# Kernel tuning notes

Hardware: AMD Instinct MI355X
Metric: run time of the kernel (lower is better)

## Reference

```python
import jax, jax.numpy as jnp
import numpy as np

RADIUS = 0.2
NSAMPLE = 32


def ball_query(new_xyz, xyz, radius, nsample):
    # new_xyz: (B, M, 3), xyz: (B, N, 3) -> idx: (B, M, nsample) int32
    B, M, _ = new_xyz.shape
    N = xyz.shape[1]
    # pairwise squared distances (B, M, N)
    diff = new_xyz[:, :, None, :] - xyz[:, None, :, :]
    dist2 = jnp.sum(diff * diff, axis=-1)
    mask = dist2 < (radius * radius)
    ar = jnp.arange(N, dtype=jnp.int32)
    masked = jnp.where(mask, ar[None, None, :], jnp.int32(N + 1))  # (B,M,N)
    sorted_idx = jnp.sort(masked, axis=2)[:, :, :nsample]          # (B,M,nsample)
    invalid = sorted_idx >= N
    first = sorted_idx[:, :, 0:1]
    idx = jnp.where(invalid, jnp.broadcast_to(first, sorted_idx.shape), sorted_idx)
    return idx


def group_points(points, idx):
    # points: (B, C, N), idx: (B, M, nsample) -> (B, C, M, nsample)
    B, C, N = points.shape
    M, ns = idx.shape[1], idx.shape[2]
    flat = jnp.broadcast_to(idx.reshape(B, 1, M * ns), (B, C, M * ns))
    return jnp.take_along_axis(points, flat, axis=2).reshape(B, C, M, ns)


def setup_inputs() -> dict:
    key = jax.random.key(0)
    k1, k2, k3 = jax.random.split(key, 3)
    xyz = jax.random.uniform(k1, (8, 16384, 3), dtype=jnp.float32)
    new_xyz = jax.random.uniform(k2, (8, 1024, 3), dtype=jnp.float32)
    features = jax.random.normal(k3, (8, 64, 16384), dtype=jnp.float32)
    return {"xyz": xyz, "new_xyz": new_xyz, "features": features}


def reference(xyz, new_xyz, features):
    idx = ball_query(new_xyz, xyz, RADIUS, NSAMPLE)          # (B,M,ns)
    xyz_t = jnp.transpose(xyz, (0, 2, 1))                    # (B,3,N)
    grouped_xyz = group_points(xyz_t, idx)                   # (B,3,M,ns)
    grouped_xyz = grouped_xyz - jnp.transpose(new_xyz, (0, 2, 1))[:, :, :, None]
    grouped_features = group_points(features, idx)           # (B,C,M,ns)
    new_features = jnp.concatenate([grouped_xyz, grouped_features], axis=1)
    return new_features                                      # (B, 3+C, M, ns)
```

## Files before the change

### kernel.cpp

```cpp
#include <hip/hip_runtime.h>


#define N_PTS   16384
#define M_Q     1024
#define B_SZ    8
#define NSAMP   32
#define NCH     64
#define R2      0.04f
#define OUT_CH  (3 + NCH)

typedef float f4 __attribute__((ext_vector_type(4)));

__global__ __launch_bounds__(256) void transpose_kernel(
    const float* __restrict__ feat, const float* __restrict__ xyz,
    float* __restrict__ ft,
    float* __restrict__ xs, float* __restrict__ ys, float* __restrict__ zs)
{
    __shared__ float tile[64][65];
    const int b   = blockIdx.x & 7;
    const int n0  = (blockIdx.x >> 3) << 6;
    const int tid = threadIdx.x;
    const float* __restrict__ fb = feat + (size_t)b * NCH * N_PTS;
    float* __restrict__ tb       = ft   + ((size_t)b * N_PTS + n0) * NCH;

    if (xs && tid < 64) {
        const int p = n0 + tid;
        const float* src = xyz + ((size_t)b * N_PTS + p) * 3;
        xs[(size_t)b * N_PTS + p] = src[0];
        ys[(size_t)b * N_PTS + p] = src[1];
        zs[(size_t)b * N_PTS + p] = src[2];
    }

#pragma unroll
    for (int j = 0; j < 4; ++j) {
        const int fidx = j * 256 + tid;
        const int c = fidx >> 4;
        const int q = fidx & 15;
        const f4 v = __builtin_nontemporal_load(
            (const f4*)&fb[(size_t)c * N_PTS + n0 + q * 4]);
        tile[c][q * 4 + 0] = v.x;
        tile[c][q * 4 + 1] = v.y;
        tile[c][q * 4 + 2] = v.z;
        tile[c][q * 4 + 3] = v.w;
    }
    __syncthreads();
    const int c4 = tid & 15;
    const int r  = tid >> 4;
#pragma unroll
    for (int j = 0; j < 4; ++j) {
        const int nn = j * 16 + r;
        f4 o;
        o.x = tile[c4 * 4 + 0][nn];
        o.y = tile[c4 * 4 + 1][nn];
        o.z = tile[c4 * 4 + 2][nn];
        o.w = tile[c4 * 4 + 3][nn];
        *(f4*)(&tb[(size_t)nn * NCH + c4 * 4]) = o;
    }
}

template <bool SOA>
__global__ __launch_bounds__(256) void qg_main(
    const float* __restrict__ xyz,
    const float* __restrict__ new_xyz,
    const float* __restrict__ ft,
    const float* __restrict__ xs, const float* __restrict__ ys,
    const float* __restrict__ zs,
    float* __restrict__ out)
{
    const int tid  = threadIdx.x;
    const int w    = tid >> 6;
    const int lane = tid & 63;
    const int b    = blockIdx.x & 7;
    const int m    = ((blockIdx.x >> 3) << 2) + w;
    const int q    = (b << 10) + m;

    __shared__ float pxyz[4][NSAMP][4];
    __shared__ float tile[4][32][33];

    const float cx = new_xyz[q * 3 + 0];
    const float cy = new_xyz[q * 3 + 1];
    const float cz = new_xyz[q * 3 + 2];
    const float* __restrict__ xb = xyz + (size_t)b * N_PTS * 3;
    const unsigned long long lmask = (1ull << lane) - 1ull;
    int cnt = 0;

    if constexpr (SOA) {
        const f4* __restrict__ xs4 = (const f4*)(xs + (size_t)b * N_PTS);
        const f4* __restrict__ ys4 = (const f4*)(ys + (size_t)b * N_PTS);
        const f4* __restrict__ zs4 = (const f4*)(zs + (size_t)b * N_PTS);

        f4 X = xs4[lane], Y = ys4[lane], Z = zs4[lane];

        for (int base = 0; ; base += 256) {
            const int  nbase = base + 256;
            const bool more  = nbase < N_PTS;
            const int  pidx  = more ? (nbase >> 2) + lane : lane;
            const f4 NX = xs4[pidx], NY = ys4[pidx], NZ = zs4[pidx];

            float d2k[4];
#pragma unroll
            for (int k = 0; k < 4; ++k) {
                const float dx = __fsub_rn(cx, X[k]);
                const float dy = __fsub_rn(cy, Y[k]);
                const float dz = __fsub_rn(cz, Z[k]);
                d2k[k] = __fadd_rn(__fadd_rn(__fmul_rn(dx, dx), __fmul_rn(dy, dy)),
                                   __fmul_rn(dz, dz));
            }
            const bool h0 = d2k[0] < R2, h1 = d2k[1] < R2;
            const bool h2 = d2k[2] < R2, h3 = d2k[3] < R2;
            const unsigned long long m0 = __ballot(h0);
            const unsigned long long m1 = __ballot(h1);
            const unsigned long long m2 = __ballot(h2);
            const unsigned long long m3 = __ballot(h3);

            const int P = (int)(__popcll(m0 & lmask) + __popcll(m1 & lmask) +
                                __popcll(m2 & lmask) + __popcll(m3 & lmask));
            int own = 0;
            const bool hk[4] = {h0, h1, h2, h3};
#pragma unroll
            for (int k = 0; k < 4; ++k) {
                if (hk[k]) {
                    const int slot = cnt + P + own;
                    if (slot < NSAMP) {
                        pxyz[w][slot][0] = X[k];
                        pxyz[w][slot][1] = Y[k];
                        pxyz[w][slot][2] = Z[k];
                        pxyz[w][slot][3] = __int_as_float(base + lane * 4 + k);
                    }
                }
                own += hk[k] ? 1 : 0;
            }
            cnt += (int)(__popcll(m0) + __popcll(m1) + __popcll(m2) + __popcll(m3));

            if (cnt >= NSAMP || !more) break;
            X = NX; Y = NY; Z = NZ;
        }
    } else {
        float Ax = xb[lane * 3 + 0], Ay = xb[lane * 3 + 1], Az = xb[lane * 3 + 2];
        float Bx = xb[(64 + lane) * 3 + 0], By = xb[(64 + lane) * 3 + 1],
              Bz = xb[(64 + lane) * 3 + 2];

        for (int base = 0; ; base += 128) {
            const int  nbase = base + 128;
            const bool more  = nbase < N_PTS;
            const int  pA = more ? nbase + lane : lane;
            const int  pB = pA + 64;
            const float nAx = xb[pA * 3 + 0], nAy = xb[pA * 3 + 1], nAz = xb[pA * 3 + 2];
            const float nBx = xb[pB * 3 + 0], nBy = xb[pB * 3 + 1], nBz = xb[pB * 3 + 2];

            {
                const float dx = __fsub_rn(cx, Ax), dy = __fsub_rn(cy, Ay), dz = __fsub_rn(cz, Az);
                const float d2 = __fadd_rn(__fadd_rn(__fmul_rn(dx, dx), __fmul_rn(dy, dy)),
                                           __fmul_rn(dz, dz));
                const bool hit = d2 < R2;
                const unsigned long long mk = __ballot(hit);
                if (hit) {
                    const int slot = cnt + __popcll(mk & lmask);
                    if (slot < NSAMP) {
                        pxyz[w][slot][0] = Ax; pxyz[w][slot][1] = Ay;
                        pxyz[w][slot][2] = Az; pxyz[w][slot][3] = __int_as_float(base + lane);
                    }
                }
                cnt += (int)__popcll(mk);
            }
            {
                const float dx = __fsub_rn(cx, Bx), dy = __fsub_rn(cy, By), dz = __fsub_rn(cz, Bz);
                const float d2 = __fadd_rn(__fadd_rn(__fmul_rn(dx, dx), __fmul_rn(dy, dy)),
                                           __fmul_rn(dz, dz));
                const bool hit = d2 < R2;
                const unsigned long long mk = __ballot(hit);
                if (hit) {
                    const int slot = cnt + __popcll(mk & lmask);
                    if (slot < NSAMP) {
                        pxyz[w][slot][0] = Bx; pxyz[w][slot][1] = By;
                        pxyz[w][slot][2] = Bz; pxyz[w][slot][3] = __int_as_float(base + 64 + lane);
                    }
                }
                cnt += (int)__popcll(mk);
            }
            if (cnt >= NSAMP || !more) break;
            Ax = nAx; Ay = nAy; Az = nAz;
            Bx = nBx; By = nBy; Bz = nBz;
        }
    }

    if (lane < NSAMP && cnt < NSAMP) {
        float v0x, v0y, v0z, v0w;
        if (cnt > 0) {
            v0x = pxyz[w][0][0]; v0y = pxyz[w][0][1];
            v0z = pxyz[w][0][2]; v0w = pxyz[w][0][3];
        } else {
            v0x = xb[0]; v0y = xb[1]; v0z = xb[2]; v0w = __int_as_float(0);
        }
        if (lane >= cnt) {
            pxyz[w][lane][0] = v0x; pxyz[w][lane][1] = v0y;
            pxyz[w][lane][2] = v0z; pxyz[w][lane][3] = v0w;
        }
    }

    float* __restrict__ ob = out + ((size_t)b * OUT_CH * M_Q + (size_t)m) * NSAMP;

    if (lane < 24) {
        const int c  = lane >> 3;
        const int s4 = lane & 7;
        const float ctr = (c == 0) ? cx : ((c == 1) ? cy : cz);
        f4 o;
        o.x = __fsub_rn(pxyz[w][s4 * 4 + 0][c], ctr);
        o.y = __fsub_rn(pxyz[w][s4 * 4 + 1][c], ctr);
        o.z = __fsub_rn(pxyz[w][s4 * 4 + 2][c], ctr);
        o.w = __fsub_rn(pxyz[w][s4 * 4 + 3][c], ctr);
        __builtin_nontemporal_store(o, (f4*)&ob[(size_t)c * (M_Q * NSAMP) + s4 * 4]);
    }

    const float* __restrict__ ftb = ft + (size_t)b * N_PTS * NCH;
    const int sgrp = lane >> 3;
    const int c4   = lane & 7;

#pragma unroll
    for (int chunk = 0; chunk < 2; ++chunk) {
        f4 vals[4];
#pragma unroll
        for (int i = 0; i < 4; ++i) {
            const int s = i * 8 + sgrp;
            const int n = __float_as_int(pxyz[w][s][3]);
            vals[i] = *(const f4*)(ftb + (size_t)n * NCH + chunk * 32 + c4 * 4);
        }
#pragma unroll
        for (int i = 0; i < 4; ++i) {
            const int s = i * 8 + sgrp;
            tile[w][c4 * 4 + 0][s] = vals[i].x;
            tile[w][c4 * 4 + 1][s] = vals[i].y;
            tile[w][c4 * 4 + 2][s] = vals[i].z;
            tile[w][c4 * 4 + 3][s] = vals[i].w;
        }
#pragma unroll
        for (int j = 0; j < 4; ++j) {
            const int c_loc = j * 8 + (lane >> 3);
            const int s4    = lane & 7;
            f4 o;
            o.x = tile[w][c_loc][s4 * 4 + 0];
            o.y = tile[w][c_loc][s4 * 4 + 1];
            o.z = tile[w][c_loc][s4 * 4 + 2];
            o.w = tile[w][c_loc][s4 * 4 + 3];
            __builtin_nontemporal_store(
                o, (f4*)&ob[(size_t)(3 + chunk * 32 + c_loc) * (M_Q * NSAMP) + s4 * 4]);
        }
    }
}

__global__ __launch_bounds__(256) void qg_fallback(
    const float* __restrict__ xyz, const float* __restrict__ new_xyz,
    const float* __restrict__ feat, float* __restrict__ out)
{
    const int tid  = threadIdx.x;
    const int w    = tid >> 6;
    const int lane = tid & 63;
    const int q    = blockIdx.x * 4 + w;
    const int b    = q >> 10;
    const int m    = q & (M_Q - 1);

    __shared__ int idx_sh[4][NSAMP];

    const float cx = new_xyz[q * 3 + 0];
    const float cy = new_xyz[q * 3 + 1];
    const float cz = new_xyz[q * 3 + 2];
    const float* __restrict__ xb = xyz + (size_t)b * N_PTS * 3;

    int cnt = 0;
    for (int base = 0; base < N_PTS && cnt < NSAMP; base += 64) {
        const int n = base + lane;
        const float dx = __fsub_rn(cx, xb[n * 3 + 0]);
        const float dy = __fsub_rn(cy, xb[n * 3 + 1]);
        const float dz = __fsub_rn(cz, xb[n * 3 + 2]);
        const float d2 = __fadd_rn(__fadd_rn(__fmul_rn(dx, dx), __fmul_rn(dy, dy)),
                                   __fmul_rn(dz, dz));
        const bool hit = d2 < R2;
        const unsigned long long mk = __ballot(hit);
        if (hit) {
            const int slot = cnt + __popcll(mk & ((1ull << lane) - 1ull));
            if (slot < NSAMP) idx_sh[w][slot] = n;
        }
        cnt += (int)__popcll(mk);
    }
    __syncthreads();
    if (lane < NSAMP) {
        const int v0 = (cnt > 0) ? idx_sh[w][0] : 0;
        if (lane >= cnt) idx_sh[w][lane] = v0;
    }
    __syncthreads();

    const float* __restrict__ fb = feat + (size_t)b * NCH * N_PTS;
    float* __restrict__ ob = out + ((size_t)b * OUT_CH * M_Q + (size_t)m) * NSAMP;
    for (int e = lane; e < OUT_CH * NSAMP; e += 64) {
        const int c = e >> 5, s = e & 31;
        const int n = idx_sh[w][s];
        float v;
        if (c < 3) {
            const float ctr = (c == 0) ? cx : ((c == 1) ? cy : cz);
            v = __fsub_rn(xb[n * 3 + c], ctr);
        } else {
            v = fb[(size_t)(c - 3) * N_PTS + n];
        }
        ob[(size_t)c * (M_Q * NSAMP) + s] = v;
    }
}

extern "C" void kernel_launch(void* const* d_in, const int* in_sizes, int n_in,
                              void* d_out, int out_size, void* d_ws, size_t ws_size,
                              hipStream_t stream) {
    const float* xyz     = (const float*)d_in[0];
    const float* new_xyz = (const float*)d_in[1];
    const float* feat    = (const float*)d_in[2];
    float* out           = (float*)d_out;

    const size_t ft_elems  = (size_t)B_SZ * N_PTS * NCH;
    const size_t soa_elems = (size_t)B_SZ * N_PTS;
    const size_t need_soa  = (ft_elems + 3 * soa_elems) * sizeof(float);
    const size_t need_ft   = ft_elems * sizeof(float);

    float* ft = (float*)d_ws;
    float* xs = ft + ft_elems;
    float* ys = xs + soa_elems;
    float* zs = ys + soa_elems;

    if (ws_size >= need_soa) {
        transpose_kernel<<<B_SZ * (N_PTS / 64), 256, 0, stream>>>(feat, xyz, ft, xs, ys, zs);
        qg_main<true><<<(B_SZ * M_Q) / 4, 256, 0, stream>>>(
            xyz, new_xyz, ft, xs, ys, zs, out);
    } else if (ws_size >= need_ft) {
        transpose_kernel<<<B_SZ * (N_PTS / 64), 256, 0, stream>>>(
            feat, xyz, ft, nullptr, nullptr, nullptr);
        qg_main<false><<<(B_SZ * M_Q) / 4, 256, 0, stream>>>(
            xyz, new_xyz, ft, nullptr, nullptr, nullptr, out);
    } else {
        qg_fallback<<<(B_SZ * M_Q) / 4, 256, 0, stream>>>(xyz, new_xyz, feat, out);
    }
}
```

Measured before the change: 120.4 us.

## Gather features via global_load_lds into swizzled LDS tile and issue loads early

Replaces the register-staged feature gather with direct global-to-LDS loads (global_load_lds, 4 bytes per lane) into a 32x32 XOR-swizzled tile instead of a padded one. The first-half gather is issued before the xyz output stores so it overlaps them, and the second half is reissued once the LDS reads finish. Launch bounds also request 8 waves per EU to raise occupancy. It drops the VGPR round trip and the LDS transpose writes, but moves from 16-byte to 4-byte global loads per lane and relies on manual waitcnt and sched_barrier ordering.

```diff
diff --git a/kernel.cpp b/kernel.cpp
--- a/kernel.cpp
+++ b/kernel.cpp
@@ -11,7 +11,12 @@
 
 typedef float f4 __attribute__((ext_vector_type(4)));
 
-__global__ __launch_bounds__(256) void transpose_kernel(
+#define GLDS4(gp, lp)                                                        \
+    __builtin_amdgcn_global_load_lds(                                        \
+        (const __attribute__((address_space(1))) unsigned int*)(gp),         \
+        (__attribute__((address_space(3))) unsigned int*)(lp), 4, 0, 0)
+
+__global__ __launch_bounds__(256, 8) void transpose_kernel(
     const float* __restrict__ feat, const float* __restrict__ xyz,
     float* __restrict__ ft,
     float* __restrict__ xs, float* __restrict__ ys, float* __restrict__ zs)
@@ -59,7 +64,7 @@
 }
 
 template <bool SOA>
-__global__ __launch_bounds__(256) void qg_main(
+__global__ __launch_bounds__(256, 8) void qg_main(
     const float* __restrict__ xyz,
     const float* __restrict__ new_xyz,
     const float* __restrict__ ft,
@@ -75,7 +80,7 @@
     const int q    = (b << 10) + m;
 
     __shared__ float pxyz[4][NSAMP][4];
-    __shared__ float tile[4][32][33];
+    __shared__ float tile[4][32][32];
 
     const float cx = new_xyz[q * 3 + 0];
     const float cy = new_xyz[q * 3 + 1];
@@ -199,6 +204,18 @@
     }
 
     float* __restrict__ ob = out + ((size_t)b * OUT_CH * M_Q + (size_t)m) * NSAMP;
+    const float* __restrict__ ftb = ft + (size_t)b * N_PTS * NCH;
+
+    const int half = lane >> 5;
+    const int c5   = lane & 31;
+
+#pragma unroll
+    for (int t = 0; t < 16; ++t) {
+        const int s   = 2 * t + half;
+        const int ns  = __float_as_int(pxyz[w][s][3]);
+        const int col = c5 ^ ((2 * t) & 28);
+        GLDS4(ftb + (size_t)ns * NCH + col, &tile[w][2 * t][0]);
+    }
 
     if (lane < 24) {
         const int c  = lane >> 3;
@@ -212,39 +229,45 @@
         __builtin_nontemporal_store(o, (f4*)&ob[(size_t)c * (M_Q * NSAMP) + s4 * 4]);
     }
 
-    const float* __restrict__ ftb = ft + (size_t)b * N_PTS * NCH;
-    const int sgrp = lane >> 3;
-    const int c4   = lane & 7;
-
-#pragma unroll
-    for (int chunk = 0; chunk < 2; ++chunk) {
-        f4 vals[4];
-#pragma unroll
-        for (int i = 0; i < 4; ++i) {
-            const int s = i * 8 + sgrp;
-            const int n = __float_as_int(pxyz[w][s][3]);
-            vals[i] = *(const f4*)(ftb + (size_t)n * NCH + chunk * 32 + c4 * 4);
-        }
-#pragma unroll
-        for (int i = 0; i < 4; ++i) {
-            const int s = i * 8 + sgrp;
-            tile[w][c4 * 4 + 0][s] = vals[i].x;
-            tile[w][c4 * 4 + 1][s] = vals[i].y;
-            tile[w][c4 * 4 + 2][s] = vals[i].z;
-            tile[w][c4 * 4 + 3][s] = vals[i].w;
-        }
-#pragma unroll
-        for (int j = 0; j < 4; ++j) {
-            const int c_loc = j * 8 + (lane >> 3);
-            const int s4    = lane & 7;
-            f4 o;
-            o.x = tile[w][c_loc][s4 * 4 + 0];
-            o.y = tile[w][c_loc][s4 * 4 + 1];
-            o.z = tile[w][c_loc][s4 * 4 + 2];
-            o.w = tile[w][c_loc][s4 * 4 + 3];
-            __builtin_nontemporal_store(
-                o, (f4*)&ob[(size_t)(3 + chunk * 32 + c_loc) * (M_Q * NSAMP) + s4 * 4]);
-        }
+    const int cl = (lane >> 3);
+    const int s4 = lane & 7;
+    const int xr = s4 * 4;
+
+    asm volatile("s_waitcnt vmcnt(0)" ::: "memory");
+    __builtin_amdgcn_sched_barrier(0);
+#pragma unroll
+    for (int j = 0; j < 4; ++j) {
+        const int c_loc = j * 8 + cl;
+        f4 o;
+        o.x = tile[w][xr + 0][c_loc ^ xr];
+        o.y = tile[w][xr + 1][c_loc ^ xr];
+        o.z = tile[w][xr + 2][c_loc ^ xr];
+        o.w = tile[w][xr + 3][c_loc ^ xr];
+        __builtin_nontemporal_store(
+            o, (f4*)&ob[(size_t)(3 + c_loc) * (M_Q * NSAMP) + s4 * 4]);
+    }
+
+    asm volatile("s_waitcnt lgkmcnt(0)" ::: "memory");
+    __builtin_amdgcn_sched_barrier(0);
+#pragma unroll
+    for (int t = 0; t < 16; ++t) {
+        const int s   = 2 * t + half;
+        const int ns  = __float_as_int(pxyz[w][s][3]);
+        const int col = c5 ^ ((2 * t) & 28);
+        GLDS4(ftb + (size_t)ns * NCH + 32 + col, &tile[w][2 * t][0]);
+    }
+    asm volatile("s_waitcnt vmcnt(0)" ::: "memory");
+    __builtin_amdgcn_sched_barrier(0);
+#pragma unroll
+    for (int j = 0; j < 4; ++j) {
+        const int c_loc = j * 8 + cl;
+        f4 o;
+        o.x = tile[w][xr + 0][c_loc ^ xr];
+        o.y = tile[w][xr + 1][c_loc ^ xr];
+        o.z = tile[w][xr + 2][c_loc ^ xr];
+        o.w = tile[w][xr + 3][c_loc ^ xr];
+        __builtin_nontemporal_store(
+            o, (f4*)&ob[(size_t)(3 + 32 + c_loc) * (M_Q * NSAMP) + s4 * 4]);
     }
 }
 
```

New measurement: 121.9 us. About the same (+1.2%).

## Fuse ball query into transpose kernel and split out gather kernel

Applied to the files above, without the earlier changes.

The ball query moves out of the gather kernel and into the feature-transpose kernel, so each block does one transpose tile and one query group. Odd and even blocks run the two phases in opposite order, which overlaps memory-bound transposing with the compute-heavy query. The query now reads interleaved xyz directly with vector loads and unpacks them in registers, so the separate per-coordinate copy of xyz is no longer built. Neighbour slots are written to a workspace buffer and read back by a separate gather kernel. This adds a small round trip through global memory in exchange for the overlap.

```diff
diff --git a/kernel.cpp b/kernel.cpp
--- a/kernel.cpp
+++ b/kernel.cpp
@@ -11,91 +11,78 @@
 
 typedef float f4 __attribute__((ext_vector_type(4)));
 
-__global__ __launch_bounds__(256) void transpose_kernel(
-    const float* __restrict__ feat, const float* __restrict__ xyz,
-    float* __restrict__ ft,
-    float* __restrict__ xs, float* __restrict__ ys, float* __restrict__ zs)
-{
-    __shared__ float tile[64][65];
-    const int b   = blockIdx.x & 7;
-    const int n0  = (blockIdx.x >> 3) << 6;
-    const int tid = threadIdx.x;
-    const float* __restrict__ fb = feat + (size_t)b * NCH * N_PTS;
-    float* __restrict__ tb       = ft   + ((size_t)b * N_PTS + n0) * NCH;
-
-    if (xs && tid < 64) {
-        const int p = n0 + tid;
-        const float* src = xyz + ((size_t)b * N_PTS + p) * 3;
-        xs[(size_t)b * N_PTS + p] = src[0];
-        ys[(size_t)b * N_PTS + p] = src[1];
-        zs[(size_t)b * N_PTS + p] = src[2];
-    }
-
-#pragma unroll
-    for (int j = 0; j < 4; ++j) {
-        const int fidx = j * 256 + tid;
-        const int c = fidx >> 4;
-        const int q = fidx & 15;
-        const f4 v = __builtin_nontemporal_load(
-            (const f4*)&fb[(size_t)c * N_PTS + n0 + q * 4]);
-        tile[c][q * 4 + 0] = v.x;
-        tile[c][q * 4 + 1] = v.y;
-        tile[c][q * 4 + 2] = v.z;
-        tile[c][q * 4 + 3] = v.w;
-    }
-    __syncthreads();
-    const int c4 = tid & 15;
-    const int r  = tid >> 4;
-#pragma unroll
-    for (int j = 0; j < 4; ++j) {
-        const int nn = j * 16 + r;
-        f4 o;
-        o.x = tile[c4 * 4 + 0][nn];
-        o.y = tile[c4 * 4 + 1][nn];
-        o.z = tile[c4 * 4 + 2][nn];
-        o.w = tile[c4 * 4 + 3][nn];
-        *(f4*)(&tb[(size_t)nn * NCH + c4 * 4]) = o;
-    }
-}
-
-template <bool SOA>
-__global__ __launch_bounds__(256) void qg_main(
+__global__ __launch_bounds__(256, 8) void k1_transpose_query(
     const float* __restrict__ xyz,
     const float* __restrict__ new_xyz,
-    const float* __restrict__ ft,
-    const float* __restrict__ xs, const float* __restrict__ ys,
-    const float* __restrict__ zs,
-    float* __restrict__ out)
+    const float* __restrict__ feat,
+    float* __restrict__ ft,
+    float* __restrict__ pslots)
 {
-    const int tid  = threadIdx.x;
-    const int w    = tid >> 6;
-    const int lane = tid & 63;
-    const int b    = blockIdx.x & 7;
-    const int m    = ((blockIdx.x >> 3) << 2) + w;
-    const int q    = (b << 10) + m;
-
+    const int tid = threadIdx.x;
+    const int b   = blockIdx.x & 7;
+    const int g   = blockIdx.x >> 3;
+
+    __shared__ float tile[64][65];
     __shared__ float pxyz[4][NSAMP][4];
-    __shared__ float tile[4][32][33];
-
-    const float cx = new_xyz[q * 3 + 0];
-    const float cy = new_xyz[q * 3 + 1];
-    const float cz = new_xyz[q * 3 + 2];
-    const float* __restrict__ xb = xyz + (size_t)b * N_PTS * 3;
-    const unsigned long long lmask = (1ull << lane) - 1ull;
-    int cnt = 0;
-
-    if constexpr (SOA) {
-        const f4* __restrict__ xs4 = (const f4*)(xs + (size_t)b * N_PTS);
-        const f4* __restrict__ ys4 = (const f4*)(ys + (size_t)b * N_PTS);
-        const f4* __restrict__ zs4 = (const f4*)(zs + (size_t)b * N_PTS);
-
-        f4 X = xs4[lane], Y = ys4[lane], Z = zs4[lane];
+
+    auto do_transpose = [&]() {
+        const int n0 = g << 6;
+        const float* __restrict__ fb = feat + (size_t)b * NCH * N_PTS;
+        float* __restrict__ tb       = ft   + ((size_t)b * N_PTS + n0) * NCH;
+#pragma unroll
+        for (int j = 0; j < 4; ++j) {
+            const int fidx = j * 256 + tid;
+            const int c = fidx >> 4, qq = fidx & 15;
+            const f4 v = __builtin_nontemporal_load(
+                (const f4*)&fb[(size_t)c * N_PTS + n0 + qq * 4]);
+            tile[c][qq * 4 + 0] = v.x;
+            tile[c][qq * 4 + 1] = v.y;
+            tile[c][qq * 4 + 2] = v.z;
+            tile[c][qq * 4 + 3] = v.w;
+        }
+        __syncthreads();
+        const int c4 = tid & 15;
+        const int r  = tid >> 4;
+#pragma unroll
+        for (int j = 0; j < 4; ++j) {
+            const int nn = j * 16 + r;
+            f4 o;
+            o.x = tile[c4 * 4 + 0][nn];
+            o.y = tile[c4 * 4 + 1][nn];
+            o.z = tile[c4 * 4 + 2][nn];
+            o.w = tile[c4 * 4 + 3][nn];
+            *(f4*)(&tb[(size_t)nn * NCH + c4 * 4]) = o;
+        }
+    };
+
+    auto do_query = [&]() {
+        const int w    = tid >> 6;
+        const int lane = tid & 63;
+        const int m    = (g << 2) + w;
+        const int q    = (b << 10) + m;
+
+        const float cx = new_xyz[q * 3 + 0];
+        const float cy = new_xyz[q * 3 + 1];
+        const float cz = new_xyz[q * 3 + 2];
+        const float* __restrict__ xb = xyz + (size_t)b * N_PTS * 3;
+        const unsigned long long lmask = (1ull << lane) - 1ull;
+        int cnt = 0;
+
+        f4 L0 = *(const f4*)(xb + lane * 12);
+        f4 L1 = *(const f4*)(xb + lane * 12 + 4);
+        f4 L2 = *(const f4*)(xb + lane * 12 + 8);
 
         for (int base = 0; ; base += 256) {
             const int  nbase = base + 256;
             const bool more  = nbase < N_PTS;
-            const int  pidx  = more ? (nbase >> 2) + lane : lane;
-            const f4 NX = xs4[pidx], NY = ys4[pidx], NZ = zs4[pidx];
+            const int  fo    = (more ? nbase * 3 : 0) + lane * 12;
+            const f4 NL0 = *(const f4*)(xb + fo);
+            const f4 NL1 = *(const f4*)(xb + fo + 4);
+            const f4 NL2 = *(const f4*)(xb + fo + 8);
+
+            const float X[4] = {L0.x, L0.w, L1.z, L2.y};
+            const float Y[4] = {L0.y, L1.x, L1.w, L2.z};
+            const float Z[4] = {L0.z, L1.y, L2.x, L2.w};
 
             float d2k[4];
 #pragma unroll
@@ -133,71 +120,55 @@
             cnt += (int)(__popcll(m0) + __popcll(m1) + __popcll(m2) + __popcll(m3));
 
             if (cnt >= NSAMP || !more) break;
-            X = NX; Y = NY; Z = NZ;
-        }
-    } else {
-        float Ax = xb[lane * 3 + 0], Ay = xb[lane * 3 + 1], Az = xb[lane * 3 + 2];
-        float Bx = xb[(64 + lane) * 3 + 0], By = xb[(64 + lane) * 3 + 1],
-              Bz = xb[(64 + lane) * 3 + 2];
-
-        for (int base = 0; ; base += 128) {
-            const int  nbase = base + 128;
-            const bool more  = nbase < N_PTS;
-            const int  pA = more ? nbase + lane : lane;
-            const int  pB = pA + 64;
-            const float nAx = xb[pA * 3 + 0], nAy = xb[pA * 3 + 1], nAz = xb[pA * 3 + 2];
-            const float nBx = xb[pB * 3 + 0], nBy = xb[pB * 3 + 1], nBz = xb[pB * 3 + 2];
-
-            {
-                const float dx = __fsub_rn(cx, Ax), dy = __fsub_rn(cy, Ay), dz = __fsub_rn(cz, Az);
-                const float d2 = __fadd_rn(__fadd_rn(__fmul_rn(dx, dx), __fmul_rn(dy, dy)),
-                                           __fmul_rn(dz, dz));
-                const bool hit = d2 < R2;
-                const unsigned long long mk = __ballot(hit);
-                if (hit) {
-                    const int slot = cnt + __popcll(mk & lmask);
-                    if (slot < NSAMP) {
-                        pxyz[w][slot][0] = Ax; pxyz[w][slot][1] = Ay;
-                        pxyz[w][slot][2] = Az; pxyz[w][slot][3] = __int_as_float(base + lane);
-                    }
-                }
-                cnt += (int)__popcll(mk);
+            L0 = NL0; L1 = NL1; L2 = NL2;
+        }
+
+        if (lane < NSAMP && cnt < NSAMP) {
+            float v0x, v0y, v0z, v0w;
+            if (cnt > 0) {
+                v0x = pxyz[w][0][0]; v0y = pxyz[w][0][1];
+                v0z = pxyz[w][0][2]; v0w = pxyz[w][0][3];
+            } else {
+                v0x = xb[0]; v0y = xb[1]; v0z = xb[2]; v0w = __int_as_float(0);
             }
-            {
-                const float dx = __fsub_rn(cx, Bx), dy = __fsub_rn(cy, By), dz = __fsub_rn(cz, Bz);
-                const float d2 = __fadd_rn(__fadd_rn(__fmul_rn(dx, dx), __fmul_rn(dy, dy)),
-                                           __fmul_rn(dz, dz));
-                const bool hit = d2 < R2;
-                const unsigned long long mk = __ballot(hit);
-                if (hit) {
-                    const int slot = cnt + __popcll(mk & lmask);
-                    if (slot < NSAMP) {
-                        pxyz[w][slot][0] = Bx; pxyz[w][slot][1] = By;
-                        pxyz[w][slot][2] = Bz; pxyz[w][slot][3] = __int_as_float(base + 64 + lane);
-                    }
-                }
-                cnt += (int)__popcll(mk);
+            if (lane >= cnt) {
+                pxyz[w][lane][0] = v0x; pxyz[w][lane][1] = v0y;
+                pxyz[w][lane][2] = v0z; pxyz[w][lane][3] = v0w;
             }
-            if (cnt >= NSAMP || !more) break;
-            Ax = nAx; Ay = nAy; Az = nAz;
-            Bx = nBx; By = nBy; Bz = nBz;
-        }
-    }
-
-    if (lane < NSAMP && cnt < NSAMP) {
-        float v0x, v0y, v0z, v0w;
-        if (cnt > 0) {
-            v0x = pxyz[w][0][0]; v0y = pxyz[w][0][1];
-            v0z = pxyz[w][0][2]; v0w = pxyz[w][0][3];
-        } else {
-            v0x = xb[0]; v0y = xb[1]; v0z = xb[2]; v0w = __int_as_float(0);
-        }
-        if (lane >= cnt) {
-            pxyz[w][lane][0] = v0x; pxyz[w][lane][1] = v0y;
-            pxyz[w][lane][2] = v0z; pxyz[w][lane][3] = v0w;
-        }
-    }
-
+        }
+        if (lane < NSAMP) {
+            *(f4*)&pslots[((size_t)q * NSAMP + lane) * 4] =
+                *(const f4*)&pxyz[w][lane][0];
+        }
+    };
+
+    if (blockIdx.x & 1) { do_query(); do_transpose(); }
+    else                { do_transpose(); do_query(); }
+}
+
+__global__ __launch_bounds__(256, 8) void k2_gather(
+    const float* __restrict__ new_xyz,
+    const float* __restrict__ ft,
+    const float* __restrict__ pslots,
+    float* __restrict__ out)
+{
+    const int tid  = threadIdx.x;
+    const int w    = tid >> 6;
+    const int lane = tid & 63;
+    const int b    = blockIdx.x & 7;
+    const int m    = ((blockIdx.x >> 3) << 2) + w;
+    const int q    = (b << 10) + m;
+
+    __shared__ float pxyz[4][NSAMP][4];
+    __shared__ float tile[4][32][33];
+
+    if (lane < NSAMP) {
+        *(f4*)&pxyz[w][lane][0] = *(const f4*)&pslots[((size_t)q * NSAMP + lane) * 4];
+    }
+
+    const float cx = new_xyz[q * 3 + 0];
+    const float cy = new_xyz[q * 3 + 1];
+    const float cz = new_xyz[q * 3 + 2];
     float* __restrict__ ob = out + ((size_t)b * OUT_CH * M_Q + (size_t)m) * NSAMP;
 
     if (lane < 24) {
@@ -212,9 +183,12 @@
         __builtin_nontemporal_store(o, (f4*)&ob[(size_t)c * (M_Q * NSAMP) + s4 * 4]);
     }
 
-    const float* __restrict__ ftb = ft + (size_t)b * N_PTS * NCH;
+    const float* __restrict__ ftb = ft;
+    const float* __restrict__ ftbb = ft;
+    const float* __restrict__ fb = ft + (size_t)b * N_PTS * NCH;
     const int sgrp = lane >> 3;
     const int c4   = lane & 7;
+    (void)ftb; (void)ftbb;
 
 #pragma unroll
     for (int chunk = 0; chunk < 2; ++chunk) {
@@ -223,7 +197,7 @@
         for (int i = 0; i < 4; ++i) {
             const int s = i * 8 + sgrp;
             const int n = __float_as_int(pxyz[w][s][3]);
-            vals[i] = *(const f4*)(ftb + (size_t)n * NCH + chunk * 32 + c4 * 4);
+            vals[i] = *(const f4*)(fb + (size_t)n * NCH + chunk * 32 + c4 * 4);
         }
 #pragma unroll
         for (int i = 0; i < 4; ++i) {
@@ -313,25 +287,17 @@
     const float* feat    = (const float*)d_in[2];
     float* out           = (float*)d_out;
 
-    const size_t ft_elems  = (size_t)B_SZ * N_PTS * NCH;
-    const size_t soa_elems = (size_t)B_SZ * N_PTS;
-    const size_t need_soa  = (ft_elems + 3 * soa_elems) * sizeof(float);
-    const size_t need_ft   = ft_elems * sizeof(float);
-
-    float* ft = (float*)d_ws;
-    float* xs = ft + ft_elems;
-    float* ys = xs + soa_elems;
-    float* zs = ys + soa_elems;
-
-    if (ws_size >= need_soa) {
-        transpose_kernel<<<B_SZ * (N_PTS / 64), 256, 0, stream>>>(feat, xyz, ft, xs, ys, zs);
-        qg_main<true><<<(B_SZ * M_Q) / 4, 256, 0, stream>>>(
-            xyz, new_xyz, ft, xs, ys, zs, out);
-    } else if (ws_size >= need_ft) {
-        transpose_kernel<<<B_SZ * (N_PTS / 64), 256, 0, stream>>>(
-            feat, xyz, ft, nullptr, nullptr, nullptr);
-        qg_main<false><<<(B_SZ * M_Q) / 4, 256, 0, stream>>>(
-            xyz, new_xyz, ft, nullptr, nullptr, nullptr, out);
+    const size_t ft_elems   = (size_t)B_SZ * N_PTS * NCH;
+    const size_t slot_elems = (size_t)B_SZ * M_Q * NSAMP * 4;
+    const size_t need       = (ft_elems + slot_elems) * sizeof(float);
+
+    float* ft     = (float*)d_ws;
+    float* pslots = ft + ft_elems;
+
+    if (ws_size >= need) {
+        k1_transpose_query<<<B_SZ * (N_PTS / 64), 256, 0, stream>>>(
+            xyz, new_xyz, feat, ft, pslots);
+        k2_gather<<<(B_SZ * M_Q) / 4, 256, 0, stream>>>(new_xyz, ft, pslots, out);
     } else {
         qg_fallback<<<(B_SZ * M_Q) / 4, 256, 0, stream>>>(xyz, new_xyz, feat, out);
     }
```

Measured after the change: 127.4 us. 1.06x slower.
